# Kernel tuning notes

Measured on AMD Instinct MI355X. Metric: run time of the kernel, lower is better.

The kernel has to match this reference:

```python
import jax, jax.numpy as jnp
import numpy as np

# dims: batch, seq, model, heads, head_dim, mlp, layers, vocab, window
B, S, D, H, DH, M, L, V, W = 2, 2048, 512, 8, 64, 2048, 6, 32000, 512
EPS = 1e-6
NEG = -1e9

def _sinusoidal(max_len, d):
    # LRA common_layers sinusoidal_init (min_scale=1, max_scale=1e4)
    pe = np.zeros((max_len, d), np.float32)
    position = np.arange(max_len)[:, None].astype(np.float32)
    scale_factor = -np.log(1e4) / (d // 2 - 1)
    div_term = np.exp(np.arange(d // 2).astype(np.float32) * scale_factor)
    pe[:, : d // 2] = np.sin(position * div_term)
    pe[:, d // 2 :] = np.cos(position * div_term)
    return jnp.asarray(pe)[None]  # [1, S, D]

POS_EMB = _sinusoidal(S, D)

def _ln(x, scale, bias):
    mu = jnp.mean(x, -1, keepdims=True)
    var = jnp.mean(jnp.square(x - mu), -1, keepdims=True)
    return (x - mu) * jax.lax.rsqrt(var + EPS) * scale + bias

def setup_inputs() -> dict:
    key = jax.random.key(0)
    ks = jax.random.split(key, 16)
    def n(k, shape, s=0.02):
        return jax.random.normal(k, shape, jnp.float32) * s
    return {
        "inputs": jax.random.randint(ks[0], (B, S), 0, V),
        "emb": n(ks[1], (V, D), 1.0),          # nn.Embed normal(stddev=1)
        "wq": n(ks[2], (L, D, H, DH)),
        "wk": n(ks[3], (L, D, H, DH)),
        "wv": n(ks[4], (L, D, H, DH)),
        "wo": n(ks[5], (L, H, DH, D)),
        "ln1_s": 1.0 + n(ks[6], (L, D)),
        "ln1_b": n(ks[7], (L, D)),
        "ln2_s": 1.0 + n(ks[8], (L, D)),
        "ln2_b": n(ks[9], (L, D)),
        "w1": n(ks[10], (L, D, M)),
        "b1": n(ks[11], (L, M), 1e-6),
        "w2": n(ks[12], (L, M, D)),
        "b2": n(ks[13], (L, D), 1e-6),
        "lnf_s": 1.0 + n(ks[14], (D,)),
        "lnf_b": n(ks[15], (D,)),
    }

def reference(inputs, emb, wq, wk, wv, wo, ln1_s, ln1_b, ln2_s, ln2_b,
              w1, b1, w2, b2, lnf_s, lnf_b):
    pad = inputs > 0                                  # [B,S] padding mask
    x = emb[inputs] + POS_EMB                         # embed + sinusoidal pos
    idx = jnp.arange(S)
    band = jnp.abs(idx[:, None] - idx[None, :]) <= (W // 2)  # sliding window
    mask = band[None, None] & pad[:, None, :, None] & pad[:, None, None, :]
    attn_bias = jnp.where(mask, 0.0, NEG)             # [B,1,S,S]
    scale = 1.0 / jnp.sqrt(jnp.float32(DH))
    for l in range(L):
        # --- Longformer self-attention (pre-LN) ---
        y = _ln(x, ln1_s[l], ln1_b[l])
        q = jnp.einsum('bsd,dhk->bshk', y, wq[l]) * scale
        k = jnp.einsum('bsd,dhk->bshk', y, wk[l])
        v = jnp.einsum('bsd,dhk->bshk', y, wv[l])
        logits = jnp.einsum('bqhk,bshk->bhqs', q, k) + attn_bias
        attn = jax.nn.softmax(logits, axis=-1)
        o = jnp.einsum('bhqs,bshk->bqhk', attn, v)
        x = x + jnp.einsum('bqhk,hkd->bqd', o, wo[l])
        # --- MLP block (pre-LN) ---
        y = _ln(x, ln2_s[l], ln2_b[l])
        h = jax.nn.gelu(jnp.einsum('bsd,dm->bsm', y, w1[l]) + b1[l])
        x = x + jnp.einsum('bsm,md->bsd', h, w2[l]) + b2[l]
    return _ln(x, lnf_s, lnf_b)                       # encoder_norm -> [B,S,D]
```

## Files before the change

### kernel.cpp

```cpp
#include <hip/hip_runtime.h>
#include <hip/hip_bf16.h>
#include <math.h>

#define B_    2
#define S_    2048
#define D_    512
#define H_    8
#define DH_   64
#define M_    2048
#define L_    6

typedef float f4v __attribute__((ext_vector_type(4)));
typedef short s8v __attribute__((ext_vector_type(8)));
typedef unsigned short u16;

#define GLOAD16(gp, lp) __builtin_amdgcn_global_load_lds( \
    (const __attribute__((address_space(1))) void*)(gp),  \
    (__attribute__((address_space(3))) void*)(lp), 16, 0, 0)

__device__ __forceinline__ unsigned pack2bf(float a, float b) {
    __hip_bfloat162 t;
    t.x = __float2bfloat16(a);
    t.y = __float2bfloat16(b);
    return *(unsigned*)&t;
}
__device__ __forceinline__ s8v cvt8bf(f4v a, f4v b) {
    union { s8v s; unsigned u[4]; } r;
    r.u[0] = pack2bf(a.x, a.y); r.u[1] = pack2bf(a.z, a.w);
    r.u[2] = pack2bf(b.x, b.y); r.u[3] = pack2bf(b.z, b.w);
    return r.s;
}
__device__ __forceinline__ float bf2f(u16 u) {
    unsigned v = ((unsigned)u) << 16;
    return *(float*)&v;
}

__global__ __launch_bounds__(256) void embed_kernel(
    const int* __restrict__ tok, const float* __restrict__ emb,
    float* __restrict__ x, int* __restrict__ pad)
{
    int t = blockIdx.x;
    int s = t & (S_ - 1);
    int d = threadIdx.x;
    int tk = tok[t];
    if (d == 0) pad[t] = (tk > 0) ? 1 : 0;
    const float sf = -9.210340371976184f / 255.0f;
    float dt  = expf((float)d * sf);
    float ang = (float)s * dt;
    x[(size_t)t * D_ + d]       = emb[(size_t)tk * D_ + d]       + sinf(ang);
    x[(size_t)t * D_ + d + 256] = emb[(size_t)tk * D_ + d + 256] + cosf(ang);
}

template<bool OBF16>
__global__ __launch_bounds__(256) void ln_kernel(
    const float* __restrict__ xin, const float* __restrict__ sc,
    const float* __restrict__ bi, void* __restrict__ yout)
{
    int t = blockIdx.x;
    int d2 = threadIdx.x;
    float2 xv = *(const float2*)&xin[(size_t)t * D_ + 2 * d2];
    float ssum = xv.x + xv.y;
    float ssq  = xv.x * xv.x + xv.y * xv.y;
    #pragma unroll
    for (int m = 32; m; m >>= 1) {
        ssum += __shfl_xor(ssum, m);
        ssq  += __shfl_xor(ssq,  m);
    }
    __shared__ float smem[8];
    int wave = threadIdx.x >> 6, lane = threadIdx.x & 63;
    if (lane == 0) { smem[wave] = ssum; smem[4 + wave] = ssq; }
    __syncthreads();
    float tsum = smem[0] + smem[1] + smem[2] + smem[3];
    float tsq  = smem[4] + smem[5] + smem[6] + smem[7];
    float mu  = tsum * (1.0f / D_);
    float var = tsq * (1.0f / D_) - mu * mu;
    float r   = rsqrtf(var + 1e-6f);
    float2 sv = *(const float2*)&sc[2 * d2];
    float2 bv = *(const float2*)&bi[2 * d2];
    float ox = (xv.x - mu) * r * sv.x + bv.x;
    float oy = (xv.y - mu) * r * sv.y + bv.y;
    if (OBF16) {
        __hip_bfloat16* y = (__hip_bfloat16*)yout;
        __hip_bfloat162 p;
        p.x = __float2bfloat16(ox); p.y = __float2bfloat16(oy);
        *(__hip_bfloat162*)&y[(size_t)t * D_ + 2 * d2] = p;
    } else {
        float* y = (float*)yout;
        float2 ov; ov.x = ox; ov.y = oy;
        *(float2*)&y[(size_t)t * D_ + 2 * d2] = ov;
    }
}

__global__ __launch_bounds__(256) void transpose_cast(
    const float* __restrict__ wq, const float* __restrict__ wk,
    const float* __restrict__ wv, const float* __restrict__ wo,
    const float* __restrict__ w1, const float* __restrict__ w2,
    __hip_bfloat16* __restrict__ dst)
{
    __shared__ float tile[32][33];
    const int l = blockIdx.y;
    const int bx = blockIdx.x;
    const size_t lbase = (size_t)l * 3145728;
    const float* src; __hip_bfloat16* d; int K, N, kt, nt;
    float wscale = 1.0f;
    if (bx < 1024) {
        int m = bx >> 8, t = bx & 255;
        const float* s4 = (m == 0) ? wq : (m == 1) ? wk : (m == 2) ? wv : wo;
        if (m == 0) wscale = 0.125f;
        src = s4 + (size_t)l * 262144;
        d = dst + lbase + (size_t)m * 262144;
        K = 512; N = 512; kt = t >> 4; nt = t & 15;
    } else if (bx < 2048) {
        int t = bx - 1024;
        src = w1 + (size_t)l * 1048576;
        d = dst + lbase + 1048576;
        K = 512; N = 2048; kt = t >> 6; nt = t & 63;
    } else {
        int t = bx - 2048;
        src = w2 + (size_t)l * 1048576;
        d = dst + lbase + 2097152;
        K = 2048; N = 512; kt = t >> 4; nt = t & 15;
    }
    const int x = threadIdx.x & 31, y = threadIdx.x >> 5;
    const int kk0 = kt * 32, nn0 = nt * 32;
    #pragma unroll
    for (int p = 0; p < 4; ++p)
        tile[y + p * 8][x] = src[(size_t)(kk0 + y + p * 8) * N + nn0 + x];
    __syncthreads();
    #pragma unroll
    for (int p = 0; p < 4; ++p)
        d[(size_t)(nn0 + y + p * 8) * K + kk0 + x] =
            __float2bfloat16(tile[x][y + p * 8] * wscale);
}

__device__ __forceinline__ float gelu_tanh(float xx) {
    float u = fminf(fmaxf(xx, -10.f), 10.f);
    float t = 0.7978845608028654f * (u + 0.044715f * u * u * u);
    float e = __expf(2.f * t);
    float th = 1.f - 2.f * __builtin_amdgcn_rcpf(e + 1.f);
    return 0.5f * xx * (1.f + th);
}

template<bool OUT_BF16>
__global__ __launch_bounds__(512) void gemm_sk(
    const __hip_bfloat16* __restrict__ A, const __hip_bfloat16* __restrict__ Wt,
    const float* __restrict__ bias, const float* __restrict__ resid,
    void* __restrict__ Cout, int K, int ldc, int ncol, int gelu)
{
    __shared__ __align__(16) char lds[73728];

    const int nwg = gridDim.x;
    const int cpx = nwg >> 3;
    const int bid = blockIdx.x;
    const int pos = (bid & 7) * cpx + (bid >> 3);
    const int row0 = (pos / ncol) * 128;
    const int col0 = (pos % ncol) * 64;

    const int tid = threadIdx.x, lane = tid & 63, w = tid >> 6;
    const int kg = w >> 2, w4 = w & 3;
    const int wr = w4 >> 1, wc = w4 & 1;
    const int lq = lane & 15, g = lane >> 4;

    const int Khalf = K >> 1;
    const int nt = Khalf >> 5;
    const char* Ab = (const char*)A;
    const char* Bt = (const char*)Wt;
    const int ldsrow = lane >> 2;
    const int swzseg = (lane & 3) ^ ((lane >> 3) & 3);
    const int slot8  = (g ^ ((lq >> 1) & 3)) * 8;

    f4v acc[4][2] = {};

    auto STAGE = [&](int c, int t) {
        const int k0 = kg * Khalf + t * 32;
        char* dst = lds + kg * 36864 + c * 12288;
        #pragma unroll
        for (int i2 = 0; i2 < 2; ++i2) {
            int seg = w4 * 2 + i2;
            const char* gp = Ab + ((size_t)(row0 + seg * 16 + ldsrow) * K + k0) * 2 + swzseg * 16;
            GLOAD16(gp, dst + seg * 1024);
        }
        {
            const char* gp = Bt + ((size_t)(col0 + w4 * 16 + ldsrow) * K + k0) * 2 + swzseg * 16;
            GLOAD16(gp, dst + 8192 + w4 * 1024);
        }
    };

    STAGE(0, 0);
    STAGE(1, 1);
    STAGE(2, 2);

    for (int t = 0; t < nt; ++t) {
        if (t < nt - 2)      asm volatile("s_waitcnt vmcnt(6)" ::: "memory");
        else if (t < nt - 1) asm volatile("s_waitcnt vmcnt(3)" ::: "memory");
        else                 asm volatile("s_waitcnt vmcnt(0)" ::: "memory");
        __builtin_amdgcn_s_barrier();
        __builtin_amdgcn_sched_barrier(0);

        const unsigned short* Al = (const unsigned short*)(lds + kg * 36864 + (t % 3) * 12288);
        const unsigned short* Bl = Al + 4096;
        s8v af[4], bfv[2];
        #pragma unroll
        for (int mi = 0; mi < 4; ++mi)
            af[mi] = *(const s8v*)&Al[(wr * 64 + mi * 16 + lq) * 32 + slot8];
        #pragma unroll
        for (int ni = 0; ni < 2; ++ni)
            bfv[ni] = *(const s8v*)&Bl[(wc * 32 + ni * 16 + lq) * 32 + slot8];

        __builtin_amdgcn_s_setprio(1);
        #pragma unroll
        for (int mi = 0; mi < 4; ++mi)
            #pragma unroll
            for (int ni = 0; ni < 2; ++ni)
                acc[mi][ni] = __builtin_amdgcn_mfma_f32_16x16x32_bf16(af[mi], bfv[ni], acc[mi][ni], 0, 0, 0);
        __builtin_amdgcn_s_setprio(0);

        asm volatile("s_waitcnt lgkmcnt(0)" ::: "memory");
        __builtin_amdgcn_s_barrier();
        __builtin_amdgcn_sched_barrier(0);
        if (t + 3 < nt) STAGE(t % 3, t + 3);
    }

    float* scr = (float*)lds;
    if (kg == 1) {
        #pragma unroll
        for (int mi = 0; mi < 4; ++mi)
            #pragma unroll
            for (int ni = 0; ni < 2; ++ni)
                *(f4v*)&scr[(((mi * 2 + ni) * 256 + w4 * 64 + lane)) * 4] = acc[mi][ni];
    }
    __syncthreads();
    if (kg == 1) return;

    #pragma unroll
    for (int mi = 0; mi < 4; ++mi)
        #pragma unroll
        for (int ni = 0; ni < 2; ++ni)
            acc[mi][ni] += *(const f4v*)&scr[(((mi * 2 + ni) * 256 + w4 * 64 + lane)) * 4];

    #pragma unroll
    for (int mi = 0; mi < 4; ++mi) {
        #pragma unroll
        for (int ni = 0; ni < 2; ++ni) {
            #pragma unroll
            for (int jj = 0; jj < 4; ++jj) {
                int rrow = row0 + wr * 64 + mi * 16 + g * 4 + jj;
                int ccol = col0 + wc * 32 + ni * 16 + lq;
                float vv = acc[mi][ni][jj];
                if (bias)  vv += bias[ccol];
                if (gelu)  vv = gelu_tanh(vv);
                if (resid) vv += resid[(size_t)rrow * ldc + ccol];
                if (OUT_BF16)
                    ((__hip_bfloat16*)Cout)[(size_t)rrow * ldc + ccol] = __float2bfloat16(vv);
                else
                    ((float*)Cout)[(size_t)rrow * ldc + ccol] = vv;
            }
        }
    }
}

__global__ __launch_bounds__(512) void attn_mfma_kernel(
    const u16* __restrict__ qkv, const int* __restrict__ pad,
    __hip_bfloat16* __restrict__ o)
{
    __shared__ __align__(16) unsigned short Klds[2][64 * 64];
    __shared__ __align__(16) unsigned short Vt[2][64 * 64];
    __shared__ float padfa[640];

    const int qt = blockIdx.x, bh = blockIdx.y;
    const int h = bh & 7, b = bh >> 3;
    const int q0 = qt * 128;
    const int tid = threadIdx.x, w = tid >> 6, lane = tid & 63;
    const int lq = lane & 15, g = lane >> 4;
    const int wq0 = q0 + w * 16;
    const size_t base = (size_t)b * S_ * 1536 + h * 64;

    for (int j = tid; j < 640; j += 512) {
        int krow = q0 - 256 + j;
        padfa[j] = (krow >= 0 && krow < S_ && pad[b * S_ + krow] != 0) ? 1.f : 0.f;
    }

    s8v qf[2];
    {
        const u16* qr = qkv + base + (size_t)(wq0 + lq) * 1536;
        #pragma unroll
        for (int ks = 0; ks < 2; ++ks)
            qf[ks] = *(const s8v*)&qr[ks * 32 + g * 8];
    }

    float lsum = 0.f;
    f4v oacc[4] = {};
    const int oblane = 256 + 4 * g - wq0 - lq;

    const int ki = tid >> 3, kss = tid & 7;
    const int vd = tid & 63, vkb = tid >> 6;
    s8v kreg;
    u16 vreg0, vreg1, vreg2, vreg3, vreg4, vreg5, vreg6, vreg7;

    auto LOAD_REGS = [&](int c) {
        const int kc = q0 - 256 + c * 64;
        {
            int krow = kc + ki;
            int kcl = krow < 0 ? 0 : (krow >= S_ ? S_ - 1 : krow);
            kreg = *(const s8v*)&qkv[base + 512 + (size_t)kcl * 1536 + kss * 8];
        }
        {
            int kr0 = kc + vkb * 8;
            const u16* vp = qkv + base + 1024 + vd;
            int c0 = kr0+0 < 0 ? 0 : (kr0+0 >= S_ ? S_-1 : kr0+0);
            int c1 = kr0+1 < 0 ? 0 : (kr0+1 >= S_ ? S_-1 : kr0+1);
            int c2 = kr0+2 < 0 ? 0 : (kr0+2 >= S_ ? S_-1 : kr0+2);
            int c3 = kr0+3 < 0 ? 0 : (kr0+3 >= S_ ? S_-1 : kr0+3);
            int c4 = kr0+4 < 0 ? 0 : (kr0+4 >= S_ ? S_-1 : kr0+4);
            int c5 = kr0+5 < 0 ? 0 : (kr0+5 >= S_ ? S_-1 : kr0+5);
            int c6 = kr0+6 < 0 ? 0 : (kr0+6 >= S_ ? S_-1 : kr0+6);
            int c7 = kr0+7 < 0 ? 0 : (kr0+7 >= S_ ? S_-1 : kr0+7);
            vreg0 = vp[(size_t)c0 * 1536]; vreg1 = vp[(size_t)c1 * 1536];
            vreg2 = vp[(size_t)c2 * 1536]; vreg3 = vp[(size_t)c3 * 1536];
            vreg4 = vp[(size_t)c4 * 1536]; vreg5 = vp[(size_t)c5 * 1536];
            vreg6 = vp[(size_t)c6 * 1536]; vreg7 = vp[(size_t)c7 * 1536];
        }
    };
    auto WRITE_LDS = [&](int buf) {
        *(s8v*)&Klds[buf][ki * 64 + ((kss ^ (ki & 7)) * 8)] = kreg;
        union { s8v s; u16 u[8]; } vv;
        vv.u[0] = vreg0; vv.u[1] = vreg1; vv.u[2] = vreg2; vv.u[3] = vreg3;
        vv.u[4] = vreg4; vv.u[5] = vreg5; vv.u[6] = vreg6; vv.u[7] = vreg7;
        *(s8v*)&Vt[buf][vd * 64 + ((vkb ^ (vd & 7)) * 8)] = vv.s;
    };

    LOAD_REGS(0);
    WRITE_LDS(0);
    LOAD_REGS(1);

    #pragma unroll 1
    for (int c = 0; c < 10; ++c) {
        asm volatile("s_waitcnt lgkmcnt(0)" ::: "memory");
        __builtin_amdgcn_s_barrier();
        __builtin_amdgcn_sched_barrier(0);
        const int kc = q0 - 256 + c * 64;
        const int buf = c & 1;

        #pragma unroll
        for (int sub = 0; sub < 2; ++sub) {
            const int kc2 = kc + sub * 32;
            if (kc2 + 31 < wq0 - 256 || kc2 > wq0 + 271) continue;

            f4v st[2] = {};
            __builtin_amdgcn_s_setprio(1);
            #pragma unroll
            for (int tt = 0; tt < 2; ++tt) {
                #pragma unroll
                for (int ks = 0; ks < 2; ++ks) {
                    const int row = sub * 32 + tt * 16 + lq;
                    const s8v af = *(const s8v*)&Klds[buf][row * 64 + (((ks * 4 + g) ^ (row & 7)) * 8)];
                    st[tt] = __builtin_amdgcn_mfma_f32_16x16x32_bf16(af, qf[ks], st[tt], 0, 0, 0);
                }
            }
            __builtin_amdgcn_s_setprio(0);

            float psum = 0.f;
            unsigned wpk[2][2];
            #pragma unroll
            for (int tt = 0; tt < 2; ++tt) {
                float pr[4];
                #pragma unroll
                for (int r = 0; r < 4; ++r) {
                    const int off = kc2 + 16 * tt + r + oblane;
                    float e = __expf(fminf(st[tt][r], 60.f)) *
                              padfa[c * 64 + sub * 32 + 16 * tt + 4 * g + r];
                    pr[r] = ((unsigned)off <= 512u) ? e : 0.f;
                    psum += pr[r];
                }
                wpk[tt][0] = pack2bf(pr[0], pr[1]);
                wpk[tt][1] = pack2bf(pr[2], pr[3]);
            }
            psum += __shfl_xor(psum, 16);
            psum += __shfl_xor(psum, 32);
            lsum += psum;

            const int srcA = (((2 * g) & 3) * 16 + lq) << 2;
            const int srcB = (((2 * g + 1) & 3) * 16 + lq) << 2;
            const bool hi = (g >= 2);
            union { s8v s; int u[4]; } pa;
            {
                int a0 = __builtin_amdgcn_ds_bpermute(srcA, (int)wpk[0][0]);
                int a1 = __builtin_amdgcn_ds_bpermute(srcA, (int)wpk[1][0]);
                pa.u[0] = hi ? a1 : a0;
                int b0 = __builtin_amdgcn_ds_bpermute(srcA, (int)wpk[0][1]);
                int b1 = __builtin_amdgcn_ds_bpermute(srcA, (int)wpk[1][1]);
                pa.u[1] = hi ? b1 : b0;
                int c0 = __builtin_amdgcn_ds_bpermute(srcB, (int)wpk[0][0]);
                int c1 = __builtin_amdgcn_ds_bpermute(srcB, (int)wpk[1][0]);
                pa.u[2] = hi ? c1 : c0;
                int d0 = __builtin_amdgcn_ds_bpermute(srcB, (int)wpk[0][1]);
                int d1 = __builtin_amdgcn_ds_bpermute(srcB, (int)wpk[1][1]);
                pa.u[3] = hi ? d1 : d0;
            }

            __builtin_amdgcn_s_setprio(1);
            #pragma unroll
            for (int dt = 0; dt < 4; ++dt) {
                const int row = dt * 16 + lq;
                const s8v vf = *(const s8v*)&Vt[buf][row * 64 + (((sub * 4 + g) ^ (row & 7)) * 8)];
                oacc[dt] = __builtin_amdgcn_mfma_f32_16x16x32_bf16(pa.s, vf, oacc[dt], 0, 0, 0);
            }
            __builtin_amdgcn_s_setprio(0);
        }

        if (c + 1 < 10) WRITE_LDS((c + 1) & 1);
        if (c + 2 < 10) LOAD_REGS(c + 2);
    }

    float inv = 1.0f / lsum;
    #pragma unroll
    for (int r = 0; r < 4; ++r) {
        int iv = __builtin_amdgcn_ds_bpermute((4 * g + r) << 2, __float_as_int(inv));
        float invq = __int_as_float(iv);
        const int qq = wq0 + 4 * g + r;
        __hip_bfloat16* orow = o + ((size_t)b * S_ + qq) * 512 + h * 64;
        #pragma unroll
        for (int dt = 0; dt < 4; ++dt)
            orow[dt * 16 + lq] = __float2bfloat16(oacc[dt][r] * invq);
    }

    {
        int padq = pad[b * S_ + wq0 + lq];
        unsigned long long bal = __ballot(g == 0 && padq == 0);
        if (bal) {
            #pragma unroll 1
            for (int r = 0; r < 16; ++r) {
                if (!((bal >> r) & 1ull)) continue;
                const int qq = wq0 + r;
                const float qd = bf2f(qkv[base + (size_t)qq * 1536 + lane]);
                float ls = 0.f, av = 0.f;
                #pragma unroll 1
                for (int s = 0; s < S_; ++s) {
                    float xp = qd * bf2f(qkv[base + 512 + (size_t)s * 1536 + lane]);
                    #pragma unroll
                    for (int m = 32; m; m >>= 1) xp += __shfl_xor(xp, m);
                    float p = __expf(fminf(xp, 60.f));
                    ls += p;
                    av += p * bf2f(qkv[base + 1024 + (size_t)s * 1536 + lane]);
                }
                o[((size_t)b * S_ + qq) * 512 + h * 64 + lane] = __float2bfloat16(av / ls);
            }
        }
    }
}

extern "C" void kernel_launch(void* const* d_in, const int* in_sizes, int n_in,
                              void* d_out, int out_size, void* d_ws, size_t ws_size,
                              hipStream_t stream)
{
    const int*   tok   = (const int*)  d_in[0];
    const float* emb   = (const float*)d_in[1];
    const float* wq    = (const float*)d_in[2];
    const float* wk    = (const float*)d_in[3];
    const float* wv    = (const float*)d_in[4];
    const float* wo    = (const float*)d_in[5];
    const float* ln1_s = (const float*)d_in[6];
    const float* ln1_b = (const float*)d_in[7];
    const float* ln2_s = (const float*)d_in[8];
    const float* ln2_b = (const float*)d_in[9];
    const float* w1    = (const float*)d_in[10];
    const float* b1    = (const float*)d_in[11];
    const float* w2    = (const float*)d_in[12];
    const float* b2    = (const float*)d_in[13];
    const float* lnf_s = (const float*)d_in[14];
    const float* lnf_b = (const float*)d_in[15];
    float* out = (float*)d_out;

    char* ws = (char*)d_ws;
    float*          x     = (float*)(ws + 0);
    __hip_bfloat16* ybf   = (__hip_bfloat16*)(ws + 8388608);
    __hip_bfloat16* qkvbf = (__hip_bfloat16*)(ws + 12582912);
    __hip_bfloat16* ob    = (__hip_bfloat16*)(ws + 37748736);
    __hip_bfloat16* hb    = (__hip_bfloat16*)(ws + 41943040);
    int*            pad   = (int*)(ws + 58720256);
    __hip_bfloat16* wT    = (__hip_bfloat16*)(ws + 58736640);

    const int NT = B_ * S_;

    transpose_cast<<<dim3(3072, L_), 256, 0, stream>>>(wq, wk, wv, wo, w1, w2, wT);
    embed_kernel<<<NT, 256, 0, stream>>>(tok, emb, x, pad);

    for (int l = 0; l < L_; ++l) {
        __hip_bfloat16* wTl = wT + (size_t)l * 3145728;
        ln_kernel<true><<<NT, 256, 0, stream>>>(x, ln1_s + l * D_, ln1_b + l * D_, (void*)ybf);
        gemm_sk<true><<<768, 512, 0, stream>>>(ybf, wTl, nullptr, nullptr,
                                               (void*)qkvbf, 512, 1536, 24, 0);
        attn_mfma_kernel<<<dim3(16, 16), 512, 0, stream>>>((const u16*)qkvbf, pad, ob);
        gemm_sk<false><<<256, 512, 0, stream>>>(ob, wTl + 786432, nullptr, x,
                                                (void*)x, 512, 512, 8, 0);
        ln_kernel<true><<<NT, 256, 0, stream>>>(x, ln2_s + l * D_, ln2_b + l * D_, (void*)ybf);
        gemm_sk<true><<<1024, 512, 0, stream>>>(ybf, wTl + 1048576, b1 + l * M_, nullptr,
                                                (void*)hb, 512, 2048, 32, 1);
        gemm_sk<false><<<256, 512, 0, stream>>>(hb, wTl + 2097152, b2 + l * D_, x,
                                                (void*)x, 2048, 512, 8, 0);
    }
    ln_kernel<false><<<NT, 256, 0, stream>>>(x, lnf_s, lnf_b, (void*)out);
}
```

Before: 748.7 us.

## Use 4-way intra-block split-K for the small-N output GEMMs

```diff
diff --git a/kernel.cpp b/kernel.cpp
--- a/kernel.cpp
+++ b/kernel.cpp
@@ -23,12 +23,6 @@
     t.x = __float2bfloat16(a);
     t.y = __float2bfloat16(b);
     return *(unsigned*)&t;
-}
-__device__ __forceinline__ s8v cvt8bf(f4v a, f4v b) {
-    union { s8v s; unsigned u[4]; } r;
-    r.u[0] = pack2bf(a.x, a.y); r.u[1] = pack2bf(a.z, a.w);
-    r.u[2] = pack2bf(b.x, b.y); r.u[3] = pack2bf(b.z, b.w);
-    return r.s;
 }
 __device__ __forceinline__ float bf2f(u16 u) {
     unsigned v = ((unsigned)u) << 16;
@@ -141,13 +135,18 @@
     return 0.5f * xx * (1.f + th);
 }
 
-template<bool OUT_BF16>
+template<int KG, bool OUT_BF16, int TAG>
 __global__ __launch_bounds__(512) void gemm_sk(
     const __hip_bfloat16* __restrict__ A, const __hip_bfloat16* __restrict__ Wt,
     const float* __restrict__ bias, const float* __restrict__ resid,
     void* __restrict__ Cout, int K, int ldc, int ncol, int gelu)
 {
-    __shared__ __align__(16) char lds[73728];
+    constexpr int WPG = 8 / KG;
+    constexpr int NI  = (KG == 2) ? 2 : 4;
+    constexpr int ASEG = 8 / WPG;
+    constexpr int BSEG = 4 / WPG;
+    constexpr int LPS  = ASEG + BSEG;
+    __shared__ __align__(16) char lds[KG * 3 * 12288];
 
     const int nwg = gridDim.x;
     const int cpx = nwg >> 3;
@@ -157,32 +156,35 @@
     const int col0 = (pos % ncol) * 64;
 
     const int tid = threadIdx.x, lane = tid & 63, w = tid >> 6;
-    const int kg = w >> 2, w4 = w & 3;
-    const int wr = w4 >> 1, wc = w4 & 1;
+    const int kg = w / WPG, wg = w % WPG;
+    const int wr = (KG == 2) ? (wg >> 1) : wg;
+    const int wc = (KG == 2) ? (wg & 1) : 0;
     const int lq = lane & 15, g = lane >> 4;
 
-    const int Khalf = K >> 1;
-    const int nt = Khalf >> 5;
+    const int Kpart = K / KG;
+    const int nt = Kpart >> 5;
     const char* Ab = (const char*)A;
     const char* Bt = (const char*)Wt;
     const int ldsrow = lane >> 2;
     const int swzseg = (lane & 3) ^ ((lane >> 3) & 3);
     const int slot8  = (g ^ ((lq >> 1) & 3)) * 8;
 
-    f4v acc[4][2] = {};
+    f4v acc[4][NI] = {};
 
     auto STAGE = [&](int c, int t) {
-        const int k0 = kg * Khalf + t * 32;
-        char* dst = lds + kg * 36864 + c * 12288;
-        #pragma unroll
-        for (int i2 = 0; i2 < 2; ++i2) {
-            int seg = w4 * 2 + i2;
+        const int k0 = kg * Kpart + t * 32;
+        char* dst = lds + (kg * 3 + c) * 12288;
+        #pragma unroll
+        for (int i2 = 0; i2 < ASEG; ++i2) {
+            int seg = wg * ASEG + i2;
             const char* gp = Ab + ((size_t)(row0 + seg * 16 + ldsrow) * K + k0) * 2 + swzseg * 16;
             GLOAD16(gp, dst + seg * 1024);
         }
-        {
-            const char* gp = Bt + ((size_t)(col0 + w4 * 16 + ldsrow) * K + k0) * 2 + swzseg * 16;
-            GLOAD16(gp, dst + 8192 + w4 * 1024);
+        #pragma unroll
+        for (int i2 = 0; i2 < BSEG; ++i2) {
+            int seg = wg * BSEG + i2;
+            const char* gp = Bt + ((size_t)(col0 + seg * 16 + ldsrow) * K + k0) * 2 + swzseg * 16;
+            GLOAD16(gp, dst + 8192 + seg * 1024);
         }
     };
 
@@ -191,27 +193,33 @@
     STAGE(2, 2);
 
     for (int t = 0; t < nt; ++t) {
-        if (t < nt - 2)      asm volatile("s_waitcnt vmcnt(6)" ::: "memory");
-        else if (t < nt - 1) asm volatile("s_waitcnt vmcnt(3)" ::: "memory");
-        else                 asm volatile("s_waitcnt vmcnt(0)" ::: "memory");
+        if (t < nt - 2) {
+            if constexpr (KG == 2) asm volatile("s_waitcnt vmcnt(6)" ::: "memory");
+            else                   asm volatile("s_waitcnt vmcnt(12)" ::: "memory");
+        } else if (t < nt - 1) {
+            if constexpr (KG == 2) asm volatile("s_waitcnt vmcnt(3)" ::: "memory");
+            else                   asm volatile("s_waitcnt vmcnt(6)" ::: "memory");
+        } else {
+            asm volatile("s_waitcnt vmcnt(0)" ::: "memory");
+        }
         __builtin_amdgcn_s_barrier();
         __builtin_amdgcn_sched_barrier(0);
 
-        const unsigned short* Al = (const unsigned short*)(lds + kg * 36864 + (t % 3) * 12288);
+        const unsigned short* Al = (const unsigned short*)(lds + (kg * 3 + t % 3) * 12288);
         const unsigned short* Bl = Al + 4096;
-        s8v af[4], bfv[2];
+        s8v af[4], bfv[NI];
         #pragma unroll
         for (int mi = 0; mi < 4; ++mi)
             af[mi] = *(const s8v*)&Al[(wr * 64 + mi * 16 + lq) * 32 + slot8];
         #pragma unroll
-        for (int ni = 0; ni < 2; ++ni)
+        for (int ni = 0; ni < NI; ++ni)
             bfv[ni] = *(const s8v*)&Bl[(wc * 32 + ni * 16 + lq) * 32 + slot8];
 
         __builtin_amdgcn_s_setprio(1);
         #pragma unroll
         for (int mi = 0; mi < 4; ++mi)
             #pragma unroll
-            for (int ni = 0; ni < 2; ++ni)
+            for (int ni = 0; ni < NI; ++ni)
                 acc[mi][ni] = __builtin_amdgcn_mfma_f32_16x16x32_bf16(af[mi], bfv[ni], acc[mi][ni], 0, 0, 0);
         __builtin_amdgcn_s_setprio(0);
 
@@ -222,26 +230,28 @@
     }
 
     float* scr = (float*)lds;
-    if (kg == 1) {
+    if (kg >= 1) {
         #pragma unroll
         for (int mi = 0; mi < 4; ++mi)
             #pragma unroll
-            for (int ni = 0; ni < 2; ++ni)
-                *(f4v*)&scr[(((mi * 2 + ni) * 256 + w4 * 64 + lane)) * 4] = acc[mi][ni];
+            for (int ni = 0; ni < NI; ++ni)
+                *(f4v*)&scr[(kg - 1) * 8192 + (((mi * NI + ni) * WPG + wg) * 64 + lane) * 4] = acc[mi][ni];
     }
     __syncthreads();
-    if (kg == 1) return;
+    if (kg >= 1) return;
 
     #pragma unroll
-    for (int mi = 0; mi < 4; ++mi)
-        #pragma unroll
-        for (int ni = 0; ni < 2; ++ni)
-            acc[mi][ni] += *(const f4v*)&scr[(((mi * 2 + ni) * 256 + w4 * 64 + lane)) * 4];
+    for (int kgi = 1; kgi < KG; ++kgi)
+        #pragma unroll
+        for (int mi = 0; mi < 4; ++mi)
+            #pragma unroll
+            for (int ni = 0; ni < NI; ++ni)
+                acc[mi][ni] += *(const f4v*)&scr[(kgi - 1) * 8192 + (((mi * NI + ni) * WPG + wg) * 64 + lane) * 4];
 
     #pragma unroll
     for (int mi = 0; mi < 4; ++mi) {
         #pragma unroll
-        for (int ni = 0; ni < 2; ++ni) {
+        for (int ni = 0; ni < NI; ++ni) {
             #pragma unroll
             for (int jj = 0; jj < 4; ++jj) {
                 int rrow = row0 + wr * 64 + mi * 16 + g * 4 + jj;
@@ -488,16 +498,16 @@
     for (int l = 0; l < L_; ++l) {
         __hip_bfloat16* wTl = wT + (size_t)l * 3145728;
         ln_kernel<true><<<NT, 256, 0, stream>>>(x, ln1_s + l * D_, ln1_b + l * D_, (void*)ybf);
-        gemm_sk<true><<<768, 512, 0, stream>>>(ybf, wTl, nullptr, nullptr,
-                                               (void*)qkvbf, 512, 1536, 24, 0);
+        gemm_sk<2, true, 0><<<768, 512, 0, stream>>>(ybf, wTl, nullptr, nullptr,
+                                                     (void*)qkvbf, 512, 1536, 24, 0);
         attn_mfma_kernel<<<dim3(16, 16), 512, 0, stream>>>((const u16*)qkvbf, pad, ob);
-        gemm_sk<false><<<256, 512, 0, stream>>>(ob, wTl + 786432, nullptr, x,
-                                                (void*)x, 512, 512, 8, 0);
+        gemm_sk<4, false, 1><<<256, 512, 0, stream>>>(ob, wTl + 786432, nullptr, x,
+                                                      (void*)x, 512, 512, 8, 0);
         ln_kernel<true><<<NT, 256, 0, stream>>>(x, ln2_s + l * D_, ln2_b + l * D_, (void*)ybf);
-        gemm_sk<true><<<1024, 512, 0, stream>>>(ybf, wTl + 1048576, b1 + l * M_, nullptr,
-                                                (void*)hb, 512, 2048, 32, 1);
-        gemm_sk<false><<<256, 512, 0, stream>>>(hb, wTl + 2097152, b2 + l * D_, x,
-                                                (void*)x, 2048, 512, 8, 0);
+        gemm_sk<2, true, 2><<<1024, 512, 0, stream>>>(ybf, wTl + 1048576, b1 + l * M_, nullptr,
+                                                      (void*)hb, 512, 2048, 32, 1);
+        gemm_sk<4, false, 3><<<256, 512, 0, stream>>>(hb, wTl + 2097152, b2 + l * D_, x,
+                                                      (void*)x, 2048, 512, 8, 0);
     }
     ln_kernel<false><<<NT, 256, 0, stream>>>(x, lnf_s, lnf_b, (void*)out);
 }
```

New measurement: 879.6 us. +17.5%, slower.
